# Kernel tuning notes

Hardware: AMD Instinct MI355X
Metric: run time of the kernel (lower is better)

The kernel has to match this reference:

```python
import jax, jax.numpy as jnp
import numpy as np

B, T, N, D = 32, 64, 300, 128


def setup_inputs() -> dict:
    key = jax.random.key(0)
    k1, k2, k3, k4 = jax.random.split(key, 4)
    src = jax.random.normal(k1, (B, T, N, D), dtype=jnp.float32)
    # Parameters are zeros-initialized in the original module (untrained);
    # use small random values so the reference computes nontrivial math.
    wt1 = jax.random.normal(k2, (D,), dtype=jnp.float32) * 0.1
    wt2 = jax.random.normal(k3, (N, D), dtype=jnp.float32) * 0.1
    wt3 = jax.random.normal(k4, (N,), dtype=jnp.float32) * 0.1
    return {"src": src, "wt1": wt1, "wt2": wt2, "wt3": wt3}


def reference(src, wt1, wt2, wt3):
    # src: [B, T, N, D]
    Q = jnp.einsum('btnd,d->btn', src, wt1)            # [B, T, N]
    K = jnp.einsum('n,btnd->btd', wt3, src)            # [B, T, D]
    # bilinear score: Q @ wt2 @ K^T per batch -> [B, T, T]
    scores = jnp.einsum('bqn,nd,bkd->bqk', Q, wt2, K)
    # NOTE: original applies softmax over dim=0 (the batch axis) — faithful here.
    att = jax.nn.softmax(scores, axis=0)               # [B, Tq, Tk]
    # time-mixing: 'btnd,bta->band' -> output indexed [b, a(=T), n, d]
    mixed = jnp.einsum('btnd,bta->band', src, att)     # [B, T, N, D]
    return src + mixed  # dropout = identity at eval
```

## Files before the change

kernel.cpp:

```cpp
#include <hip/hip_runtime.h>

#define Bb 32
#define Tt 64
#define Nn 300
#define Dd 128
#define NC (Nn * Dd)
#define BTND ((size_t)Tt * NC)

__global__ __launch_bounds__(256) void qk_kernel(
        const float* __restrict__ src, const float* __restrict__ wt1,
        const float* __restrict__ wt3, float* __restrict__ Q,
        float* __restrict__ K) {
    __shared__ float wt3_s[Nn];
    __shared__ float kred[8 * Dd];
    const int tid = threadIdx.x;
    const int grp = tid >> 5;
    const int gl = tid & 31;
    for (int i = tid; i < Nn; i += 256) wt3_s[i] = wt3[i];
    __syncthreads();
    const int d0 = gl * 4;
    const float4 w1 = *(const float4*)(wt1 + d0);
    const float* sbt = src + (size_t)blockIdx.x * NC;
    float* Qrow = Q + (size_t)blockIdx.x * Nn;
    float4 k = {0.f, 0.f, 0.f, 0.f};
    for (int n0 = 0; n0 < Nn; n0 += 8) {
        const int n = n0 + grp;
        if (n < Nn) {
            float4 v = *(const float4*)(sbt + n * Dd + d0);
            float q = v.x * w1.x + v.y * w1.y + v.z * w1.z + v.w * w1.w;
            #pragma unroll
            for (int off = 16; off > 0; off >>= 1) q += __shfl_down(q, off, 32);
            if (gl == 0) Qrow[n] = q;
            const float w3 = wt3_s[n];
            k.x = fmaf(w3, v.x, k.x);
            k.y = fmaf(w3, v.y, k.y);
            k.z = fmaf(w3, v.z, k.z);
            k.w = fmaf(w3, v.w, k.w);
        }
    }
    *(float4*)(kred + grp * Dd + d0) = k;
    __syncthreads();
    if (tid < Dd) {
        float s = 0.f;
        #pragma unroll
        for (int g = 0; g < 8; ++g) s += kred[g * Dd + tid];
        K[(size_t)blockIdx.x * Dd + tid] = s;
    }
}

__global__ __launch_bounds__(128) void score_kernel(
        const float* __restrict__ Q, const float* __restrict__ K,
        const float* __restrict__ wt2, float* __restrict__ scores) {
    __shared__ float qs[Nn];
    __shared__ float qws[Dd];
    const int tid = threadIdx.x;
    const int bq = blockIdx.x;
    const float* Qrow = Q + (size_t)bq * Nn;
    for (int i = tid; i < Nn; i += 128) qs[i] = Qrow[i];
    __syncthreads();
    float qw = 0.f;
    for (int n = 0; n < Nn; ++n) qw = fmaf(qs[n], wt2[n * Dd + tid], qw);
    qws[tid] = qw;
    __syncthreads();
    if (tid < Tt) {
        const int b = bq >> 6;
        const float* Krow = K + (size_t)(b * Tt + tid) * Dd;
        float s = 0.f;
        for (int d = 0; d < Dd; ++d) s = fmaf(qws[d], Krow[d], s);
        scores[(size_t)bq * Tt + tid] = s;
    }
}

__global__ __launch_bounds__(256) void softmax_b_kernel(
        const float* __restrict__ scores, float* __restrict__ att) {
    const int idx = blockIdx.x * 256 + threadIdx.x;
    float v[Bb];
    float m = -1e30f;
    #pragma unroll
    for (int b = 0; b < Bb; ++b) {
        v[b] = scores[b * (Tt * Tt) + idx];
        m = fmaxf(m, v[b]);
    }
    float sum = 0.f;
    #pragma unroll
    for (int b = 0; b < Bb; ++b) {
        float e = __expf(v[b] - m);
        v[b] = e;
        sum += e;
    }
    const float inv = 1.0f / sum;
    const float diag = (idx % 65 == 0) ? 1.0f : 0.0f;
    #pragma unroll
    for (int b = 0; b < Bb; ++b) att[b * (Tt * Tt) + idx] = v[b] * inv + diag;
}

#define MIX_JT 256
__global__ __launch_bounds__(256, 4) void mix_kernel(
        const float* __restrict__ src, const float* __restrict__ attI,
        float* __restrict__ out) {
    const int tid = threadIdx.x;
    const int b = blockIdx.y;
    const int lane = tid & 63;
    const int a0 = __builtin_amdgcn_readfirstlane((tid >> 6) * 16);
    const int j = blockIdx.x * MIX_JT + lane * 4;
    const float* sb = src + (size_t)b * BTND + j;
    float* ob = out + (size_t)b * BTND + j;
    const float* ab = attI + ((size_t)b << 12) + a0;
    float acc[16][4];
    #pragma unroll
    for (int ai = 0; ai < 16; ++ai)
        #pragma unroll
        for (int jj = 0; jj < 4; ++jj) acc[ai][jj] = 0.f;
    float4 x = *(const float4*)sb;
    for (int t = 0; t < Tt; ++t) {
        const int tn = (t < Tt - 1) ? t + 1 : t;
        const float4 xn = *(const float4*)(sb + (size_t)tn * NC);
        float av[16];
        #pragma unroll
        for (int i = 0; i < 16; ++i) av[i] = ab[t * Tt + i];
        #pragma unroll
        for (int ai = 0; ai < 16; ++ai) {
            acc[ai][0] = fmaf(av[ai], x.x, acc[ai][0]);
            acc[ai][1] = fmaf(av[ai], x.y, acc[ai][1]);
            acc[ai][2] = fmaf(av[ai], x.z, acc[ai][2]);
            acc[ai][3] = fmaf(av[ai], x.w, acc[ai][3]);
        }
        x = xn;
    }
    #pragma unroll
    for (int ai = 0; ai < 16; ++ai) {
        float4 s = {acc[ai][0], acc[ai][1], acc[ai][2], acc[ai][3]};
        *(float4*)(ob + (size_t)(a0 + ai) * NC) = s;
    }
}

extern "C" void kernel_launch(void* const* d_in, const int* in_sizes, int n_in,
                              void* d_out, int out_size, void* d_ws, size_t ws_size,
                              hipStream_t stream) {
    const float* src = (const float*)d_in[0];
    const float* wt1 = (const float*)d_in[1];
    const float* wt2 = (const float*)d_in[2];
    const float* wt3 = (const float*)d_in[3];
    float* out = (float*)d_out;

    float* ws = (float*)d_ws;
    float* Q      = ws;
    float* K      = Q + (size_t)Bb * Tt * Nn;
    float* scores = K + (size_t)Bb * Tt * Dd;
    float* att    = scores + (size_t)Bb * Tt * Tt;

    qk_kernel<<<Bb * Tt, 256, 0, stream>>>(src, wt1, wt3, Q, K);
    score_kernel<<<Bb * Tt, 128, 0, stream>>>(Q, K, wt2, scores);
    softmax_b_kernel<<<(Tt * Tt) / 256, 256, 0, stream>>>(scores, att);
    dim3 g4(NC / MIX_JT, Bb);
    mix_kernel<<<g4, 256, 0, stream>>>(src, att, out);
}
```

Baseline: 820.1 us.

## Fuse QW projection into QK pass, fuse score+softmax, stage attention in LDS

The Q·wt2 projection moves into the QK kernel, so Q never goes to global memory and 128 threads compute QW from shared Q. Score computation and the batch-axis softmax are merged into one kernel indexed by (q,k), which removes the scores buffer and one launch. The mix kernel now loads the per-batch 64x64 attention matrix into LDS and uses 512-thread blocks where each wave owns 8 output rows instead of 16. This lowers register pressure but halves the FMA reuse per loaded src element.

```diff
diff --git a/kernel.cpp b/kernel.cpp
--- a/kernel.cpp
+++ b/kernel.cpp
@@ -7,11 +7,12 @@
 #define NC (Nn * Dd)
 #define BTND ((size_t)Tt * NC)
 
-__global__ __launch_bounds__(256) void qk_kernel(
+__global__ __launch_bounds__(256) void qkw_kernel(
         const float* __restrict__ src, const float* __restrict__ wt1,
-        const float* __restrict__ wt3, float* __restrict__ Q,
-        float* __restrict__ K) {
+        const float* __restrict__ wt2, const float* __restrict__ wt3,
+        float* __restrict__ QW, float* __restrict__ K) {
     __shared__ float wt3_s[Nn];
+    __shared__ float qs[Nn];
     __shared__ float kred[8 * Dd];
     const int tid = threadIdx.x;
     const int grp = tid >> 5;
@@ -21,7 +22,6 @@
     const int d0 = gl * 4;
     const float4 w1 = *(const float4*)(wt1 + d0);
     const float* sbt = src + (size_t)blockIdx.x * NC;
-    float* Qrow = Q + (size_t)blockIdx.x * Nn;
     float4 k = {0.f, 0.f, 0.f, 0.f};
     for (int n0 = 0; n0 < Nn; n0 += 8) {
         const int n = n0 + grp;
@@ -30,7 +30,7 @@
             float q = v.x * w1.x + v.y * w1.y + v.z * w1.z + v.w * w1.w;
             #pragma unroll
             for (int off = 16; off > 0; off >>= 1) q += __shfl_down(q, off, 32);
-            if (gl == 0) Qrow[n] = q;
+            if (gl == 0) qs[n] = q;
             const float w3 = wt3_s[n];
             k.x = fmaf(w3, v.x, k.x);
             k.y = fmaf(w3, v.y, k.y);
@@ -45,81 +45,80 @@
         #pragma unroll
         for (int g = 0; g < 8; ++g) s += kred[g * Dd + tid];
         K[(size_t)blockIdx.x * Dd + tid] = s;
+        const float* w2c = wt2 + tid;
+        float qw0 = 0.f, qw1 = 0.f, qw2 = 0.f, qw3 = 0.f;
+        for (int n = 0; n < Nn; n += 4) {
+            qw0 = fmaf(qs[n + 0], w2c[(n + 0) * Dd], qw0);
+            qw1 = fmaf(qs[n + 1], w2c[(n + 1) * Dd], qw1);
+            qw2 = fmaf(qs[n + 2], w2c[(n + 2) * Dd], qw2);
+            qw3 = fmaf(qs[n + 3], w2c[(n + 3) * Dd], qw3);
+        }
+        QW[(size_t)blockIdx.x * Dd + tid] = (qw0 + qw1) + (qw2 + qw3);
     }
 }
 
-__global__ __launch_bounds__(128) void score_kernel(
-        const float* __restrict__ Q, const float* __restrict__ K,
-        const float* __restrict__ wt2, float* __restrict__ scores) {
-    __shared__ float qs[Nn];
-    __shared__ float qws[Dd];
+__global__ __launch_bounds__(128) void score_softmax_kernel(
+        const float* __restrict__ QW, const float* __restrict__ K,
+        float* __restrict__ att) {
+    __shared__ float sc[Bb];
+    const int kk = blockIdx.x, q = blockIdx.y;
     const int tid = threadIdx.x;
-    const int bq = blockIdx.x;
-    const float* Qrow = Q + (size_t)bq * Nn;
-    for (int i = tid; i < Nn; i += 128) qs[i] = Qrow[i];
+    const int bg = tid >> 5, gl = tid & 31;
+    const int d0 = gl * 4;
+    #pragma unroll
+    for (int i = 0; i < 8; ++i) {
+        const int b = bg * 8 + i;
+        const float4 qw = *(const float4*)(QW + ((size_t)b * Tt + q) * Dd + d0);
+        const float4 kv = *(const float4*)(K + ((size_t)b * Tt + kk) * Dd + d0);
+        float p = qw.x * kv.x + qw.y * kv.y + qw.z * kv.z + qw.w * kv.w;
+        #pragma unroll
+        for (int off = 16; off > 0; off >>= 1) p += __shfl_down(p, off, 32);
+        if (gl == 0) sc[b] = p;
+    }
     __syncthreads();
-    float qw = 0.f;
-    for (int n = 0; n < Nn; ++n) qw = fmaf(qs[n], wt2[n * Dd + tid], qw);
-    qws[tid] = qw;
-    __syncthreads();
-    if (tid < Tt) {
-        const int b = bq >> 6;
-        const float* Krow = K + (size_t)(b * Tt + tid) * Dd;
-        float s = 0.f;
-        for (int d = 0; d < Dd; ++d) s = fmaf(qws[d], Krow[d], s);
-        scores[(size_t)bq * Tt + tid] = s;
+    float m = -1e30f;
+    #pragma unroll
+    for (int b = 0; b < Bb; ++b) m = fmaxf(m, sc[b]);
+    float sum = 0.f;
+    #pragma unroll
+    for (int b = 0; b < Bb; ++b) sum += __expf(sc[b] - m);
+    if (tid < Bb) {
+        const float diag = (q == kk) ? 1.0f : 0.0f;
+        att[(size_t)tid * (Tt * Tt) + q * Tt + kk] =
+            __expf(sc[tid] - m) / sum + diag;
     }
 }
 
-__global__ __launch_bounds__(256) void softmax_b_kernel(
-        const float* __restrict__ scores, float* __restrict__ att) {
-    const int idx = blockIdx.x * 256 + threadIdx.x;
-    float v[Bb];
-    float m = -1e30f;
-    #pragma unroll
-    for (int b = 0; b < Bb; ++b) {
-        v[b] = scores[b * (Tt * Tt) + idx];
-        m = fmaxf(m, v[b]);
-    }
-    float sum = 0.f;
-    #pragma unroll
-    for (int b = 0; b < Bb; ++b) {
-        float e = __expf(v[b] - m);
-        v[b] = e;
-        sum += e;
-    }
-    const float inv = 1.0f / sum;
-    const float diag = (idx % 65 == 0) ? 1.0f : 0.0f;
-    #pragma unroll
-    for (int b = 0; b < Bb; ++b) att[b * (Tt * Tt) + idx] = v[b] * inv + diag;
-}
-
 #define MIX_JT 256
-__global__ __launch_bounds__(256, 4) void mix_kernel(
+__global__ __launch_bounds__(512, 6) void mix_kernel(
         const float* __restrict__ src, const float* __restrict__ attI,
         float* __restrict__ out) {
+    __shared__ float att_s[Tt * Tt];
     const int tid = threadIdx.x;
     const int b = blockIdx.y;
-    const int lane = tid & 63;
-    const int a0 = __builtin_amdgcn_readfirstlane((tid >> 6) * 16);
+    for (int i = tid; i < Tt * Tt; i += 512)
+        att_s[i] = attI[(size_t)b * Tt * Tt + i];
+    __syncthreads();
+    const int wave = tid >> 6, lane = tid & 63;
+    const int a0 = wave * 8;
     const int j = blockIdx.x * MIX_JT + lane * 4;
     const float* sb = src + (size_t)b * BTND + j;
     float* ob = out + (size_t)b * BTND + j;
-    const float* ab = attI + ((size_t)b << 12) + a0;
-    float acc[16][4];
+    float acc[8][4];
     #pragma unroll
-    for (int ai = 0; ai < 16; ++ai)
+    for (int ai = 0; ai < 8; ++ai)
         #pragma unroll
         for (int jj = 0; jj < 4; ++jj) acc[ai][jj] = 0.f;
     float4 x = *(const float4*)sb;
     for (int t = 0; t < Tt; ++t) {
         const int tn = (t < Tt - 1) ? t + 1 : t;
         const float4 xn = *(const float4*)(sb + (size_t)tn * NC);
-        float av[16];
+        const float4 av0 = *(const float4*)(att_s + t * Tt + a0);
+        const float4 av1 = *(const float4*)(att_s + t * Tt + a0 + 4);
+        const float av[8] = {av0.x, av0.y, av0.z, av0.w,
+                             av1.x, av1.y, av1.z, av1.w};
         #pragma unroll
-        for (int i = 0; i < 16; ++i) av[i] = ab[t * Tt + i];
-        #pragma unroll
-        for (int ai = 0; ai < 16; ++ai) {
+        for (int ai = 0; ai < 8; ++ai) {
             acc[ai][0] = fmaf(av[ai], x.x, acc[ai][0]);
             acc[ai][1] = fmaf(av[ai], x.y, acc[ai][1]);
             acc[ai][2] = fmaf(av[ai], x.z, acc[ai][2]);
@@ -128,7 +127,7 @@
         x = xn;
     }
     #pragma unroll
-    for (int ai = 0; ai < 16; ++ai) {
+    for (int ai = 0; ai < 8; ++ai) {
         float4 s = {acc[ai][0], acc[ai][1], acc[ai][2], acc[ai][3]};
         *(float4*)(ob + (size_t)(a0 + ai) * NC) = s;
     }
@@ -144,14 +143,13 @@
     float* out = (float*)d_out;
 
     float* ws = (float*)d_ws;
-    float* Q      = ws;
-    float* K      = Q + (size_t)Bb * Tt * Nn;
-    float* scores = K + (size_t)Bb * Tt * Dd;
-    float* att    = scores + (size_t)Bb * Tt * Tt;
+    float* QW  = ws;
+    float* K   = QW + (size_t)Bb * Tt * Dd;
+    float* att = K + (size_t)Bb * Tt * Dd;
 
-    qk_kernel<<<Bb * Tt, 256, 0, stream>>>(src, wt1, wt3, Q, K);
-    score_kernel<<<Bb * Tt, 128, 0, stream>>>(Q, K, wt2, scores);
-    softmax_b_kernel<<<(Tt * Tt) / 256, 256, 0, stream>>>(scores, att);
-    dim3 g4(NC / MIX_JT, Bb);
-    mix_kernel<<<g4, 256, 0, stream>>>(src, att, out);
+    qkw_kernel<<<Bb * Tt, 256, 0, stream>>>(src, wt1, wt2, wt3, QW, K);
+    dim3 g2(Tt, Tt);
+    score_softmax_kernel<<<g2, 128, 0, stream>>>(QW, K, att);
+    dim3 g3(NC / MIX_JT, Bb);
+    mix_kernel<<<g3, 512, 0, stream>>>(src, att, out);
 }
```

Result: faster. 657.1 us (-19.9%).
